# Kernel tuning notes

Hardware: AMD Instinct MI355X
Metric: run time of the kernel (lower is better)

Reference implementation:

```python
import jax, jax.numpy as jnp
import numpy as np

N_Q, M, D, DV = 4096, 32768, 512, 512  # groups, keys, key dim, value dim


def setup_inputs() -> dict:
    key = jax.random.key(0)
    k1, k2, k3 = jax.random.split(key, 3)
    query = jax.random.normal(k1, (N_Q, D), dtype=jnp.float32)
    keys = jax.random.normal(k2, (M, D), dtype=jnp.float32)
    values = jax.random.normal(k3, (M, DV), dtype=jnp.float32)
    # each query/group owns exactly M//N_Q keys -> no empty softmax rows
    tree_idx = jnp.arange(M, dtype=jnp.int32) % N_Q
    return {"query": query, "keys": keys, "values": values, "tree_idx": tree_idx}


def _l2_normalize(x, eps=1e-12):
    # matches F.normalize(x, dim=1, p=2): x / max(||x||_2, eps)
    n = jnp.linalg.norm(x, axis=1, keepdims=True)
    return x / jnp.maximum(n, eps)


def reference(query, keys, values, tree_idx):
    n_q = query.shape[0]
    # mask[q, m] = (tree_idx[m] == q); equivalent to zeros.index_add(0, tree_idx, eye(M)).bool()
    mask = tree_idx[None, :] == jnp.arange(n_q, dtype=tree_idx.dtype)[:, None]  # [N_q, M]
    query_n = _l2_normalize(query)
    keys_n = _l2_normalize(keys)
    align = query_n @ keys_n.T                      # [N_q, M] cosine similarities
    align = jnp.where(mask, align, -jnp.inf)        # masked_fill_(~mask, -inf)
    alpha = jax.nn.softmax(align, axis=1)           # segment-masked softmax per query
    att = alpha @ values                            # [N_q, DV]
    return att, alpha.sum(axis=0)
```

## Files before the change

kernel.cpp:

```cpp
#include <hip/hip_runtime.h>
#include <math.h>

#define D_DIM 512
#define MAXK 1024


__global__ void zero_counts(int* counts, int n) {
    int i = blockIdx.x * blockDim.x + threadIdx.x;
    if (i < n) counts[i] = 0;
}

__global__ void count_keys(const int* __restrict__ tree_idx,
                           int* __restrict__ counts, int m_total) {
    int m = blockIdx.x * blockDim.x + threadIdx.x;
    if (m < m_total) atomicAdd(&counts[tree_idx[m]], 1);
}

__global__ __launch_bounds__(1024) void scan_counts(const int* __restrict__ counts,
                                                    int* __restrict__ offsets,
                                                    int* __restrict__ cursor,
                                                    int n_q) {
    __shared__ int sh[1024];
    const int tid = threadIdx.x;
    const int items = (n_q + 1023) >> 10;
    const int base_idx = tid * items;

    int local = 0;
    for (int i = 0; i < items; ++i) {
        int idx = base_idx + i;
        if (idx < n_q) local += counts[idx];
    }
    sh[tid] = local;
    __syncthreads();
    for (int ofs = 1; ofs < 1024; ofs <<= 1) {
        int v = (tid >= ofs) ? sh[tid - ofs] : 0;
        __syncthreads();
        sh[tid] += v;
        __syncthreads();
    }
    int run = (tid == 0) ? 0 : sh[tid - 1];
    for (int i = 0; i < items; ++i) {
        int idx = base_idx + i;
        if (idx < n_q) {
            offsets[idx] = run;
            cursor[idx]  = run;
            run += counts[idx];
        }
    }
    if (tid == 1023) offsets[n_q] = sh[1023];
}

__global__ void scatter_keys(const int* __restrict__ tree_idx,
                             int* __restrict__ cursor,
                             int* __restrict__ keylist, int m_total) {
    int m = blockIdx.x * blockDim.x + threadIdx.x;
    if (m < m_total) {
        int p = atomicAdd(&cursor[tree_idx[m]], 1);
        keylist[p] = m;
    }
}


__global__ __launch_bounds__(64) void attn_segment(
        const float* __restrict__ query, const float* __restrict__ keys,
        const float* __restrict__ values, const int* __restrict__ offsets,
        const int* __restrict__ keylist, float* __restrict__ att,
        float* __restrict__ colsum) {
    const int q    = blockIdx.x;
    const int lane = threadIdx.x;
    const int off  = offsets[q];
    int nk = offsets[q + 1] - off;
    if (nk > MAXK) nk = MAXK;

    __shared__ float s_sc[MAXK];
    __shared__ int   s_m[MAXK];

    for (int j = lane; j < nk; j += 64) s_m[j] = keylist[off + j];

    const float4* qp = (const float4*)(query + (size_t)q * D_DIM);
    float4 qa = qp[lane];
    float4 qb = qp[lane + 64];
    float pq = qa.x*qa.x + qa.y*qa.y + qa.z*qa.z + qa.w*qa.w
             + qb.x*qb.x + qb.y*qb.y + qb.z*qb.z + qb.w*qb.w;
#pragma unroll
    for (int o = 32; o > 0; o >>= 1) pq += __shfl_down(pq, o);
    pq = __shfl(pq, 0);
    const float qinv = 1.0f / fmaxf(sqrtf(pq), 1e-12f);

    __syncthreads();

    for (int j = 0; j < nk; ++j) {
        const float4* kp = (const float4*)(keys + (size_t)s_m[j] * D_DIM);
        float4 ka = kp[lane];
        float4 kb = kp[lane + 64];
        float pd = qa.x*ka.x + qa.y*ka.y + qa.z*ka.z + qa.w*ka.w
                 + qb.x*kb.x + qb.y*kb.y + qb.z*kb.z + qb.w*kb.w;
        float pk = ka.x*ka.x + ka.y*ka.y + ka.z*ka.z + ka.w*ka.w
                 + kb.x*kb.x + kb.y*kb.y + kb.z*kb.z + kb.w*kb.w;
#pragma unroll
        for (int o = 32; o > 0; o >>= 1) {
            pd += __shfl_down(pd, o);
            pk += __shfl_down(pk, o);
        }
        if (lane == 0) {
            float kinv = 1.0f / fmaxf(sqrtf(pk), 1e-12f);
            s_sc[j] = pd * qinv * kinv;
        }
    }
    __syncthreads();

    float mx = -INFINITY;
    for (int j = lane; j < nk; j += 64) mx = fmaxf(mx, s_sc[j]);
#pragma unroll
    for (int o = 32; o > 0; o >>= 1) mx = fmaxf(mx, __shfl_down(mx, o));
    mx = __shfl(mx, 0);

    float sum = 0.0f;
    for (int j = lane; j < nk; j += 64) {
        float e = __expf(s_sc[j] - mx);
        s_sc[j] = e;
        sum += e;
    }
#pragma unroll
    for (int o = 32; o > 0; o >>= 1) sum += __shfl_down(sum, o);
    sum = __shfl(sum, 0);
    const float inv = (sum > 0.0f) ? 1.0f / sum : 0.0f;

    for (int j = lane; j < nk; j += 64) {
        float a = s_sc[j] * inv;
        s_sc[j] = a;
        colsum[s_m[j]] = a;
    }
    __syncthreads();

    float4 acc_a = make_float4(0.f, 0.f, 0.f, 0.f);
    float4 acc_b = make_float4(0.f, 0.f, 0.f, 0.f);
    for (int j = 0; j < nk; ++j) {
        const float a = s_sc[j];
        const float4* vp = (const float4*)(values + (size_t)s_m[j] * D_DIM);
        float4 va = vp[lane];
        float4 vb = vp[lane + 64];
        acc_a.x += a * va.x; acc_a.y += a * va.y; acc_a.z += a * va.z; acc_a.w += a * va.w;
        acc_b.x += a * vb.x; acc_b.y += a * vb.y; acc_b.z += a * vb.z; acc_b.w += a * vb.w;
    }
    float4* op = (float4*)(att + (size_t)q * D_DIM);
    op[lane]      = acc_a;
    op[lane + 64] = acc_b;
}

extern "C" void kernel_launch(void* const* d_in, const int* in_sizes, int n_in,
                              void* d_out, int out_size, void* d_ws, size_t ws_size,
                              hipStream_t stream) {
    const float* query    = (const float*)d_in[0];
    const float* keys     = (const float*)d_in[1];
    const float* values   = (const float*)d_in[2];
    const int*   tree_idx = (const int*)d_in[3];

    const int n_q     = in_sizes[0] / D_DIM;
    const int m_total = in_sizes[3];

    float* att    = (float*)d_out;
    float* colsum = att + (size_t)n_q * D_DIM;

    int* counts  = (int*)d_ws;
    int* offsets = counts + n_q;
    int* cursor  = offsets + n_q + 1;
    int* keylist = cursor + n_q;

    zero_counts<<<(n_q + 255) / 256, 256, 0, stream>>>(counts, n_q);
    count_keys<<<(m_total + 255) / 256, 256, 0, stream>>>(tree_idx, counts, m_total);
    scan_counts<<<1, 1024, 0, stream>>>(counts, offsets, cursor, n_q);
    scatter_keys<<<(m_total + 255) / 256, 256, 0, stream>>>(tree_idx, cursor, keylist, m_total);
    attn_segment<<<n_q, 64, 0, stream>>>(query, keys, values, offsets, keylist, att, colsum);
}
```

Before: 171.6 us.

## Fuse keylist build into one kernel and register-resident small-segment attention

```diff
diff --git a/kernel.cpp b/kernel.cpp
--- a/kernel.cpp
+++ b/kernel.cpp
@@ -2,148 +2,182 @@
 #include <math.h>
 
 #define D_DIM 512
-#define MAXK 1024
-
-
-__global__ void zero_counts(int* counts, int n) {
-    int i = blockIdx.x * blockDim.x + threadIdx.x;
-    if (i < n) counts[i] = 0;
-}
-
-__global__ void count_keys(const int* __restrict__ tree_idx,
-                           int* __restrict__ counts, int m_total) {
-    int m = blockIdx.x * blockDim.x + threadIdx.x;
-    if (m < m_total) atomicAdd(&counts[tree_idx[m]], 1);
-}
-
-__global__ __launch_bounds__(1024) void scan_counts(const int* __restrict__ counts,
-                                                    int* __restrict__ offsets,
-                                                    int* __restrict__ cursor,
-                                                    int n_q) {
-    __shared__ int sh[1024];
+
+__global__ __launch_bounds__(1024) void build_keylist(
+        const int* __restrict__ tree_idx, int m_total, int n_q,
+        int* __restrict__ offsets , int* __restrict__ keylist) {
+    extern __shared__ int lds[];
+    int* cnt  = lds;
+    int* tsum = lds + n_q;
     const int tid = threadIdx.x;
+
+    for (int i = tid; i < n_q; i += 1024) cnt[i] = 0;
+    __syncthreads();
+    for (int i = tid; i < m_total; i += 1024) atomicAdd(&cnt[tree_idx[i]], 1);
+    __syncthreads();
+
     const int items = (n_q + 1023) >> 10;
-    const int base_idx = tid * items;
-
+    const int base  = tid * items;
     int local = 0;
     for (int i = 0; i < items; ++i) {
-        int idx = base_idx + i;
-        if (idx < n_q) local += counts[idx];
-    }
-    sh[tid] = local;
-    __syncthreads();
-    for (int ofs = 1; ofs < 1024; ofs <<= 1) {
-        int v = (tid >= ofs) ? sh[tid - ofs] : 0;
+        int idx = base + i;
+        if (idx < n_q) local += cnt[idx];
+    }
+    tsum[tid] = local;
+    __syncthreads();
+    for (int o = 1; o < 1024; o <<= 1) {
+        int v = (tid >= o) ? tsum[tid - o] : 0;
         __syncthreads();
-        sh[tid] += v;
+        tsum[tid] += v;
         __syncthreads();
     }
-    int run = (tid == 0) ? 0 : sh[tid - 1];
+    int run = (tid == 0) ? 0 : tsum[tid - 1];
     for (int i = 0; i < items; ++i) {
-        int idx = base_idx + i;
+        int idx = base + i;
         if (idx < n_q) {
+            int c = cnt[idx];
             offsets[idx] = run;
-            cursor[idx]  = run;
-            run += counts[idx];
-        }
-    }
-    if (tid == 1023) offsets[n_q] = sh[1023];
+            cnt[idx] = run;
+            run += c;
+        }
+    }
+    if (tid == 1023) offsets[n_q] = tsum[1023];
+    __syncthreads();
+
+    for (int i = tid; i < m_total; i += 1024) {
+        int p = atomicAdd(&cnt[tree_idx[i]], 1);
+        keylist[p] = i;
+    }
 }
 
-__global__ void scatter_keys(const int* __restrict__ tree_idx,
-                             int* __restrict__ cursor,
-                             int* __restrict__ keylist, int m_total) {
-    int m = blockIdx.x * blockDim.x + threadIdx.x;
-    if (m < m_total) {
-        int p = atomicAdd(&cursor[tree_idx[m]], 1);
-        keylist[p] = m;
-    }
-}
-
-
-__global__ __launch_bounds__(64) void attn_segment(
+__global__ __launch_bounds__(256, 4) void attn_main(
         const float* __restrict__ query, const float* __restrict__ keys,
         const float* __restrict__ values, const int* __restrict__ offsets,
         const int* __restrict__ keylist, float* __restrict__ att,
-        float* __restrict__ colsum) {
-    const int q    = blockIdx.x;
-    const int lane = threadIdx.x;
-    const int off  = offsets[q];
-    int nk = offsets[q + 1] - off;
-    if (nk > MAXK) nk = MAXK;
-
-    __shared__ float s_sc[MAXK];
-    __shared__ int   s_m[MAXK];
-
-    for (int j = lane; j < nk; j += 64) s_m[j] = keylist[off + j];
+        float* __restrict__ colsum, int n_q) {
+    const int wave = threadIdx.x >> 6;
+    const int lane = threadIdx.x & 63;
+    const int q = (blockIdx.x << 2) + wave;
+    if (q >= n_q) return;
+
+    const int off = offsets[q];
+    const int nk  = offsets[q + 1] - off;
 
     const float4* qp = (const float4*)(query + (size_t)q * D_DIM);
     float4 qa = qp[lane];
     float4 qb = qp[lane + 64];
     float pq = qa.x*qa.x + qa.y*qa.y + qa.z*qa.z + qa.w*qa.w
              + qb.x*qb.x + qb.y*qb.y + qb.z*qb.z + qb.w*qb.w;
+
+    float4* op = (float4*)(att + (size_t)q * D_DIM);
+
+    if (nk <= 8 && nk > 0) {
+        int m[8];
+#pragma unroll
+        for (int j = 0; j < 8; ++j) m[j] = (j < nk) ? keylist[off + j] : 0;
+
+        float4 ka[8], kb[8];
+#pragma unroll
+        for (int j = 0; j < 8; ++j) {
+            const float4* kp = (const float4*)(keys + (size_t)m[j] * D_DIM);
+            ka[j] = kp[lane];
+            kb[j] = kp[lane + 64];
+        }
+
+        float pd[8], pk[8];
+#pragma unroll
+        for (int j = 0; j < 8; ++j) {
+            pd[j] = qa.x*ka[j].x + qa.y*ka[j].y + qa.z*ka[j].z + qa.w*ka[j].w
+                  + qb.x*kb[j].x + qb.y*kb[j].y + qb.z*kb[j].z + qb.w*kb[j].w;
+            pk[j] = ka[j].x*ka[j].x + ka[j].y*ka[j].y + ka[j].z*ka[j].z + ka[j].w*ka[j].w
+                  + kb[j].x*kb[j].x + kb[j].y*kb[j].y + kb[j].z*kb[j].z + kb[j].w*kb[j].w;
+        }
+
+#pragma unroll
+        for (int o = 32; o > 0; o >>= 1) {
+            pq += __shfl_down(pq, o);
+#pragma unroll
+            for (int j = 0; j < 8; ++j) {
+                pd[j] += __shfl_down(pd[j], o);
+                pk[j] += __shfl_down(pk[j], o);
+            }
+        }
+        const float qinv = 1.0f / fmaxf(sqrtf(__shfl(pq, 0)), 1e-12f);
+
+        float e[8];
+        float sum = 0.0f;
+#pragma unroll
+        for (int j = 0; j < 8; ++j) {
+            float d  = __shfl(pd[j], 0);
+            float k2 = __shfl(pk[j], 0);
+            float kinv = 1.0f / fmaxf(sqrtf(k2), 1e-12f);
+            float s = d * qinv * kinv;
+            e[j] = (j < nk) ? __expf(s) : 0.0f;
+            sum += e[j];
+        }
+        const float inv = (sum > 0.0f) ? 1.0f / sum : 0.0f;
+
+        if (lane == 0) {
+#pragma unroll
+            for (int j = 0; j < 8; ++j)
+                if (j < nk) colsum[m[j]] = e[j] * inv;
+        }
+
+        float4 acc_a = make_float4(0.f, 0.f, 0.f, 0.f);
+        float4 acc_b = make_float4(0.f, 0.f, 0.f, 0.f);
+#pragma unroll
+        for (int j = 0; j < 8; ++j) {
+            const float4* vp = (const float4*)(values + (size_t)m[j] * D_DIM);
+            float4 va = vp[lane];
+            float4 vb = vp[lane + 64];
+            float w = e[j] * inv;
+            acc_a.x += w*va.x; acc_a.y += w*va.y; acc_a.z += w*va.z; acc_a.w += w*va.w;
+            acc_b.x += w*vb.x; acc_b.y += w*vb.y; acc_b.z += w*vb.z; acc_b.w += w*vb.w;
+        }
+        op[lane]      = acc_a;
+        op[lane + 64] = acc_b;
+        return;
+    }
+
 #pragma unroll
     for (int o = 32; o > 0; o >>= 1) pq += __shfl_down(pq, o);
-    pq = __shfl(pq, 0);
-    const float qinv = 1.0f / fmaxf(sqrtf(pq), 1e-12f);
-
-    __syncthreads();
-
+    const float qinv = 1.0f / fmaxf(sqrtf(__shfl(pq, 0)), 1e-12f);
+
+    float sum = 0.0f;
     for (int j = 0; j < nk; ++j) {
-        const float4* kp = (const float4*)(keys + (size_t)s_m[j] * D_DIM);
-        float4 ka = kp[lane];
-        float4 kb = kp[lane + 64];
+        const float4* kp = (const float4*)(keys + (size_t)keylist[off + j] * D_DIM);
+        float4 ka = kp[lane], kb = kp[lane + 64];
         float pd = qa.x*ka.x + qa.y*ka.y + qa.z*ka.z + qa.w*ka.w
                  + qb.x*kb.x + qb.y*kb.y + qb.z*kb.z + qb.w*kb.w;
         float pk = ka.x*ka.x + ka.y*ka.y + ka.z*ka.z + ka.w*ka.w
                  + kb.x*kb.x + kb.y*kb.y + kb.z*kb.z + kb.w*kb.w;
 #pragma unroll
-        for (int o = 32; o > 0; o >>= 1) {
-            pd += __shfl_down(pd, o);
-            pk += __shfl_down(pk, o);
-        }
-        if (lane == 0) {
-            float kinv = 1.0f / fmaxf(sqrtf(pk), 1e-12f);
-            s_sc[j] = pd * qinv * kinv;
-        }
-    }
-    __syncthreads();
-
-    float mx = -INFINITY;
-    for (int j = lane; j < nk; j += 64) mx = fmaxf(mx, s_sc[j]);
-#pragma unroll
-    for (int o = 32; o > 0; o >>= 1) mx = fmaxf(mx, __shfl_down(mx, o));
-    mx = __shfl(mx, 0);
-
-    float sum = 0.0f;
-    for (int j = lane; j < nk; j += 64) {
-        float e = __expf(s_sc[j] - mx);
-        s_sc[j] = e;
-        sum += e;
-    }
-#pragma unroll
-    for (int o = 32; o > 0; o >>= 1) sum += __shfl_down(sum, o);
-    sum = __shfl(sum, 0);
+        for (int o = 32; o > 0; o >>= 1) { pd += __shfl_down(pd, o); pk += __shfl_down(pk, o); }
+        float d = __shfl(pd, 0), k2 = __shfl(pk, 0);
+        sum += __expf(d * qinv / fmaxf(sqrtf(k2), 1e-12f));
+    }
     const float inv = (sum > 0.0f) ? 1.0f / sum : 0.0f;
-
-    for (int j = lane; j < nk; j += 64) {
-        float a = s_sc[j] * inv;
-        s_sc[j] = a;
-        colsum[s_m[j]] = a;
-    }
-    __syncthreads();
 
     float4 acc_a = make_float4(0.f, 0.f, 0.f, 0.f);
     float4 acc_b = make_float4(0.f, 0.f, 0.f, 0.f);
     for (int j = 0; j < nk; ++j) {
-        const float a = s_sc[j];
-        const float4* vp = (const float4*)(values + (size_t)s_m[j] * D_DIM);
-        float4 va = vp[lane];
-        float4 vb = vp[lane + 64];
-        acc_a.x += a * va.x; acc_a.y += a * va.y; acc_a.z += a * va.z; acc_a.w += a * va.w;
-        acc_b.x += a * vb.x; acc_b.y += a * vb.y; acc_b.z += a * vb.z; acc_b.w += a * vb.w;
-    }
-    float4* op = (float4*)(att + (size_t)q * D_DIM);
+        const int mj = keylist[off + j];
+        const float4* kp = (const float4*)(keys + (size_t)mj * D_DIM);
+        float4 ka = kp[lane], kb = kp[lane + 64];
+        float pd = qa.x*ka.x + qa.y*ka.y + qa.z*ka.z + qa.w*ka.w
+                 + qb.x*kb.x + qb.y*kb.y + qb.z*kb.z + qb.w*kb.w;
+        float pk = ka.x*ka.x + ka.y*ka.y + ka.z*ka.z + ka.w*ka.w
+                 + kb.x*kb.x + kb.y*kb.y + kb.z*kb.z + kb.w*kb.w;
+#pragma unroll
+        for (int o = 32; o > 0; o >>= 1) { pd += __shfl_down(pd, o); pk += __shfl_down(pk, o); }
+        float d = __shfl(pd, 0), k2 = __shfl(pk, 0);
+        float a = __expf(d * qinv / fmaxf(sqrtf(k2), 1e-12f)) * inv;
+        if (lane == 0) colsum[mj] = a;
+        const float4* vp = (const float4*)(values + (size_t)mj * D_DIM);
+        float4 va = vp[lane], vb = vp[lane + 64];
+        acc_a.x += a*va.x; acc_a.y += a*va.y; acc_a.z += a*va.z; acc_a.w += a*va.w;
+        acc_b.x += a*vb.x; acc_b.y += a*vb.y; acc_b.z += a*vb.z; acc_b.w += a*vb.w;
+    }
     op[lane]      = acc_a;
     op[lane + 64] = acc_b;
 }
@@ -162,14 +196,11 @@
     float* att    = (float*)d_out;
     float* colsum = att + (size_t)n_q * D_DIM;
 
-    int* counts  = (int*)d_ws;
-    int* offsets = counts + n_q;
-    int* cursor  = offsets + n_q + 1;
-    int* keylist = cursor + n_q;
-
-    zero_counts<<<(n_q + 255) / 256, 256, 0, stream>>>(counts, n_q);
-    count_keys<<<(m_total + 255) / 256, 256, 0, stream>>>(tree_idx, counts, m_total);
-    scan_counts<<<1, 1024, 0, stream>>>(counts, offsets, cursor, n_q);
-    scatter_keys<<<(m_total + 255) / 256, 256, 0, stream>>>(tree_idx, cursor, keylist, m_total);
-    attn_segment<<<n_q, 64, 0, stream>>>(query, keys, values, offsets, keylist, att, colsum);
+    int* offsets = (int*)d_ws;
+    int* keylist = offsets + n_q + 1;
+
+    const size_t lds_bytes = (size_t)(n_q + 1024) * sizeof(int);
+    build_keylist<<<1, 1024, lds_bytes, stream>>>(tree_idx, m_total, n_q, offsets, keylist);
+    attn_main<<<(n_q + 3) / 4, 256, 0, stream>>>(query, keys, values, offsets, keylist,
+                                                 att, colsum, n_q);
 }
```

After: 195.3 us. 1.14x slower.
